# Performance work log

Measured on AMD Instinct MI355X. Metric: run time of the kernel, lower is better.

## Reference

```python
import jax, jax.numpy as jnp
import numpy as np

NEG = -1e9
SLOPE = 0.2  # LeakyReLU slope (GAT convention)


def setup_inputs() -> dict:
    key = jax.random.key(0)
    ks = jax.random.split(key, 10)
    T, N, E, F, Hd = 32, 512, 64, 64, 64
    x = jax.random.normal(ks[0], (T, N, F), dtype=jnp.float32)
    # Hyperedge incidence [N, E]; guarantee every node is in >= 1 hyperedge.
    Hm = (jax.random.uniform(ks[1], (N, E)) < (2.0 / E)).astype(jnp.int32)
    Hm = Hm.at[jnp.arange(N), jnp.arange(N) % E].set(1)
    # Industry adjacency [N, N] with self loops.
    adj = (jax.random.uniform(ks[2], (N, N)) < 0.05).astype(jnp.int32)
    adj = adj.at[jnp.arange(N), jnp.arange(N)].set(1)
    sc = 0.1
    W = jax.random.normal(ks[3], (F, Hd), jnp.float32) * sc
    a_hyp = jax.random.normal(ks[4], (Hd,), jnp.float32) * sc
    a_ind = jax.random.normal(ks[5], (Hd,), jnp.float32) * sc
    Wc1 = jax.random.normal(ks[6], (Hd, Hd), jnp.float32) * sc
    bc1 = jnp.zeros((Hd,), jnp.float32)
    wc2 = jax.random.normal(ks[7], (Hd,), jnp.float32) * sc
    bc2 = jnp.zeros((), jnp.float32)
    return dict(x=x, H=Hm, adj=adj, nhid=Hd, W=W, a_hyp=a_hyp, a_ind=a_ind,
                Wc1=Wc1, bc1=bc1, wc2=wc2, bc2=bc2)


def _edgeconv(feats, mask, Wc1, bc1, wc2, bc2):
    """Attention pooling over the second-to-last (set) axis.
    feats: [..., K, Hd], mask: broadcastable to [..., K] (bool). -> [..., Hd]"""
    z = jnp.maximum(feats @ Wc1 + bc1, 0.0) @ wc2 + bc2  # [..., K]
    z = jnp.where(mask, z, NEG)
    alpha = jax.nn.softmax(z, axis=-1)
    return jnp.einsum('...k,...kd->...d', alpha, feats)


def reference(x, H, adj, nhid, W, a_hyp, a_ind, Wc1, bc1, wc2, bc2):
    # x: [T, N, F]; H: [N, E] incidence; adj: [N, N]. Eval mode: dropout = id.
    Hb = H.astype(bool)          # [N, E]
    Ab = adj.astype(bool)        # [N, N]
    h = x @ W                    # [T, N, Hd]

    # --- hyperedge_attn: intra-hyperedge node attention (GAT-style) ---
    s_hyp = jax.nn.leaky_relu(h @ a_hyp, SLOPE)                 # [T, N]
    logits = jnp.where(Hb[None, :, :], s_hyp[:, :, None], NEG)  # [T, N, E]
    alpha = jax.nn.softmax(logits, axis=1)                      # over nodes in edge
    # per-(edge,node) contribution; original layout [E,T,N,Hd] -> here [T,N,E,Hd]
    all_hyper = jax.nn.elu(alpha[..., None] * h[:, :, None, :])  # [T, N, E, Hd]

    # --- industry attention over adj ---
    s_ind = jax.nn.leaky_relu(h @ a_ind, SLOPE)                   # [T, N]
    li = jnp.where(Ab[None, :, :], s_ind[:, None, :], NEG)        # [T, N, N]
    beta = jax.nn.softmax(li, axis=-1)
    industry = jnp.einsum('tij,tjd->tid', beta, h)                # [T, N, Hd]

    # --- per-node loop, vectorized ---
    # y8: EdgeConv over the hyperedges containing each node (mask = H row).
    # When a node has exactly 1 hyperedge, masked softmax selects it exactly,
    # which reproduces the original else-branch.
    y8 = _edgeconv(all_hyper, Hb[None, :, :], Wc1, bc1, wc2, bc2)  # [T, N, Hd]
    pair = jnp.stack([industry, y8], axis=2)                       # [T, N, 2, Hd]
    y9 = _edgeconv(pair, jnp.ones((1, 1, 2), bool), Wc1, bc1, wc2, bc2)
    return y9                                                      # [T, N, Hd]
```

## Files before the change

### kernel.cpp

```cpp
#include <hip/hip_runtime.h>

#define T_DIM 32
#define N_DIM 512
#define E_DIM 64
#define F_DIM 64
#define HD    64
#define NBR_CAP 128

static_assert(E_DIM == 64 && HD == 64 && F_DIM == 64, "wave-mapped dims");

__device__ __forceinline__ float wave_sum(float v) {
    #pragma unroll
    for (int off = 32; off > 0; off >>= 1) v += __shfl_xor(v, off, 64);
    return v;
}
__device__ __forceinline__ void wave_sum2(float& a, float& b) {
    #pragma unroll
    for (int off = 32; off > 0; off >>= 1) {
        a += __shfl_xor(a, off, 64);
        b += __shfl_xor(b, off, 64);
    }
}

#define K1_R 16
#define K1_ROWBLK (T_DIM * N_DIM / K1_R)
#define K1_CSRBLK (N_DIM / 4)
__global__ __launch_bounds__(256) void k1_h_s(
    const float* __restrict__ x, const float* __restrict__ W,
    const float* __restrict__ a_hyp, const float* __restrict__ a_ind,
    const int* __restrict__ adj, const int* __restrict__ Hm,
    float* __restrict__ h, float* __restrict__ s_hyp, float* __restrict__ s_ind,
    int* __restrict__ degs, int* __restrict__ nbrs, int* __restrict__ Ht)
{
    const int wave = threadIdx.x >> 6;
    const int lane = threadIdx.x & 63;

    if (blockIdx.x < K1_ROWBLK) {
        __shared__ float xl[K1_R * F_DIM];
        const int row0 = blockIdx.x * K1_R;
        ((float4*)xl)[threadIdx.x] =
            ((const float4*)(x + (size_t)row0 * F_DIM))[threadIdx.x];
        float wcol[F_DIM];
        #pragma unroll
        for (int f = 0; f < F_DIM; ++f) wcol[f] = W[f * HD + lane];
        const float ah = a_hyp[lane], ai = a_ind[lane];
        __syncthreads();
        #pragma unroll
        for (int r = wave; r < K1_R; r += 4) {
            float a0 = 0.f, a1 = 0.f, a2 = 0.f, a3 = 0.f;
            #pragma unroll
            for (int f = 0; f < F_DIM; f += 4) {
                const float4 xv = *(const float4*)&xl[r * F_DIM + f];
                a0 = fmaf(xv.x, wcol[f + 0], a0);
                a1 = fmaf(xv.y, wcol[f + 1], a1);
                a2 = fmaf(xv.z, wcol[f + 2], a2);
                a3 = fmaf(xv.w, wcol[f + 3], a3);
            }
            const float acc = (a0 + a1) + (a2 + a3);
            h[(size_t)(row0 + r) * HD + lane] = acc;
            float sh = acc * ah, si = acc * ai;
            wave_sum2(sh, si);
            if (lane == 0) {
                s_hyp[row0 + r] = sh > 0.f ? sh : 0.2f * sh;
                s_ind[row0 + r] = si > 0.f ? si : 0.2f * si;
            }
        }
    } else if (blockIdx.x < K1_ROWBLK + K1_CSRBLK) {
        const int i = (blockIdx.x - K1_ROWBLK) * 4 + wave;
        int deg = 0;
        #pragma unroll
        for (int c = 0; c < N_DIM / 64; ++c) {
            const int j = c * 64 + lane;
            const bool bit = adj[(size_t)i * N_DIM + j] != 0;
            const unsigned long long mask = __ballot(bit);
            if (bit) {
                const int pos = deg + __popcll(mask & ((1ull << lane) - 1ull));
                nbrs[i * NBR_CAP + pos] = j;
            }
            deg += __popcll(mask);
        }
        if (lane == 0) degs[i] = deg;
    } else {
        for (int idx = threadIdx.x; idx < N_DIM * E_DIM; idx += 256) {
            const int n = idx >> 6, e = idx & 63;
            Ht[e * N_DIM + n] = Hm[idx];
        }
    }
}

#define K2_BLOCKS (T_DIM * E_DIM / 4)
__global__ __launch_bounds__(256) void k23_stats_industry(
    const int* __restrict__ Ht, const int* __restrict__ degs,
    const int* __restrict__ nbrs,
    const float* __restrict__ s_hyp, const float* __restrict__ s_ind,
    const float* __restrict__ h,
    float* __restrict__ d_e, float* __restrict__ industry)
{
    const int wave = threadIdx.x >> 6;
    const int lane = threadIdx.x & 63;

    if (blockIdx.x < K2_BLOCKS) {
        const int idx = blockIdx.x * 4 + wave;
        const int t = idx >> 6, e = idx & 63;
        const int*   hrow = Ht + e * N_DIM;
        const float* srow = s_hyp + t * N_DIM;
        float sum = 0.f;
        #pragma unroll
        for (int c = 0; c < N_DIM / 64; ++c) {
            const int n = c * 64 + lane;
            if (hrow[n]) sum += expf(srow[n]);
        }
        sum = wave_sum(sum);
        if (lane == 0) d_e[idx] = sum;
    } else {
        const int idx = (blockIdx.x - K2_BLOCKS) * 4 + wave;
        const int t = idx >> 9, i = idx & (N_DIM - 1);
        const int deg = degs[i];
        const int* nb = nbrs + i * NBR_CAP;
        const float* st = s_ind + t * N_DIM;
        const float* hbase = h + (size_t)t * N_DIM * HD;
        float evp = 0.f, ac0 = 0.f, ac1 = 0.f, ac2 = 0.f, ac3 = 0.f;
        for (int base = 0; base < deg; base += 64) {
            const int k = base + lane;
            const bool valid = k < deg;
            const int j = valid ? nb[k] : 0;
            const float ev = valid ? expf(st[j]) : 0.f;
            evp += ev;
            const int cnt = min(deg - base, 64);
            int kk = 0;
            for (; kk + 4 <= cnt; kk += 4) {
                const int j0 = __shfl(j, kk, 64),     j1 = __shfl(j, kk + 1, 64);
                const int j2 = __shfl(j, kk + 2, 64), j3 = __shfl(j, kk + 3, 64);
                const float w0 = __shfl(ev, kk, 64),     w1 = __shfl(ev, kk + 1, 64);
                const float w2 = __shfl(ev, kk + 2, 64), w3 = __shfl(ev, kk + 3, 64);
                const float v0 = hbase[(size_t)j0 * HD + lane];
                const float v1 = hbase[(size_t)j1 * HD + lane];
                const float v2 = hbase[(size_t)j2 * HD + lane];
                const float v3 = hbase[(size_t)j3 * HD + lane];
                ac0 = fmaf(w0, v0, ac0);
                ac1 = fmaf(w1, v1, ac1);
                ac2 = fmaf(w2, v2, ac2);
                ac3 = fmaf(w3, v3, ac3);
            }
            for (; kk < cnt; ++kk) {
                const int jj = __shfl(j, kk, 64);
                const float ww = __shfl(ev, kk, 64);
                ac0 = fmaf(ww, hbase[(size_t)jj * HD + lane], ac0);
            }
        }
        const float evsum = wave_sum(evp);
        industry[(size_t)idx * HD + lane] = ((ac0 + ac1) + (ac2 + ac3)) / evsum;
    }
}

__global__ __launch_bounds__(256) void k4_final(
    const int* __restrict__ Hm, const float* __restrict__ s_hyp,
    const float* __restrict__ d_e,
    const float* __restrict__ h, const float* __restrict__ industry,
    const float* __restrict__ Wc1, const float* __restrict__ bc1,
    const float* __restrict__ wc2, const float* __restrict__ bc2,
    float* __restrict__ out)
{
    __shared__ float fl[4 * 2 * HD];
    const int wave = threadIdx.x >> 6;
    const int lane = threadIdx.x & 63;
    const int idx  = blockIdx.x * 4 + wave;
    const int t = idx >> 9, n = idx & (N_DIM - 1);
    float* fw = fl + wave * 2 * HD;

    float wreg[HD];
    #pragma unroll
    for (int d = 0; d < HD; ++d) wreg[d] = Wc1[d * HD + lane];
    const float bc1v = bc1[lane];
    const float wc2v = wc2[lane];
    const float bc2v = bc2[0];

    const float hv = h[(size_t)idx * HD + lane];
    const float esh = expf(s_hyp[idx]);

    const int memv = Hm[n * E_DIM + lane];
    const float alpha = memv ? esh * __frcp_rn(d_e[t * E_DIM + lane]) : 0.f;
    unsigned long long mk = __ballot(memv != 0);

    float zsum = 0.f, acc = 0.f;
    while (mk) {
        const int e0 = __ffsll((long long)mk) - 1; mk &= mk - 1;
        const bool have1 = mk != 0;
        const int e1 = have1 ? __ffsll((long long)mk) - 1 : e0;
        if (have1) mk &= mk - 1;
        const float a0 = __shfl(alpha, e0, 64);
        const float a1 = __shfl(alpha, e1, 64);
        float f0 = a0 * hv; f0 = f0 > 0.f ? f0 : expm1f(f0);
        float f1 = a1 * hv; f1 = f1 > 0.f ? f1 : expm1f(f1);
        fw[lane]      = f0;
        fw[HD + lane] = f1;
        float u0 = 0.f, u1 = 0.f, u2 = 0.f, u3 = 0.f;
        float v0 = 0.f, v1 = 0.f, v2 = 0.f, v3 = 0.f;
        #pragma unroll
        for (int d = 0; d < HD; d += 4) {
            const float4 A = *(const float4*)&fw[d];
            const float4 B = *(const float4*)&fw[HD + d];
            u0 = fmaf(A.x, wreg[d + 0], u0);
            u1 = fmaf(A.y, wreg[d + 1], u1);
            u2 = fmaf(A.z, wreg[d + 2], u2);
            u3 = fmaf(A.w, wreg[d + 3], u3);
            v0 = fmaf(B.x, wreg[d + 0], v0);
            v1 = fmaf(B.y, wreg[d + 1], v1);
            v2 = fmaf(B.z, wreg[d + 2], v2);
            v3 = fmaf(B.w, wreg[d + 3], v3);
        }
        float p = fmaxf((u0 + u1) + (u2 + u3) + bc1v, 0.f) * wc2v;
        float q = fmaxf((v0 + v1) + (v2 + v3) + bc1v, 0.f) * wc2v;
        wave_sum2(p, q);
        const float w0 = expf(p + bc2v);
        const float w1 = have1 ? expf(q + bc2v) : 0.f;
        zsum += w0 + w1;
        acc = fmaf(w0, f0, acc);
        acc = fmaf(w1, f1, acc);
    }
    const float y8 = acc / zsum;

    const float indv = industry[(size_t)idx * HD + lane];
    fw[lane]      = indv;
    fw[HD + lane] = y8;
    float p0 = 0.f, p1 = 0.f, q0 = 0.f, q1 = 0.f;
    #pragma unroll
    for (int d = 0; d < HD; d += 4) {
        const float4 iv = *(const float4*)&fw[d];
        const float4 yv = *(const float4*)&fw[HD + d];
        p0 = fmaf(iv.x, wreg[d + 0], p0);
        p1 = fmaf(iv.y, wreg[d + 1], p1);
        p0 = fmaf(iv.z, wreg[d + 2], p0);
        p1 = fmaf(iv.w, wreg[d + 3], p1);
        q0 = fmaf(yv.x, wreg[d + 0], q0);
        q1 = fmaf(yv.y, wreg[d + 1], q1);
        q0 = fmaf(yv.z, wreg[d + 2], q0);
        q1 = fmaf(yv.w, wreg[d + 3], q1);
    }
    float zp = fmaxf(p0 + p1 + bc1v, 0.f) * wc2v;
    float zq = fmaxf(q0 + q1 + bc1v, 0.f) * wc2v;
    wave_sum2(zp, zq);
    const float w0 = expf(zp + bc2v), w1 = expf(zq + bc2v);
    out[(size_t)idx * HD + lane] = fmaf(w0, indv, w1 * y8) / (w0 + w1);
}

extern "C" void kernel_launch(void* const* d_in, const int* in_sizes, int n_in,
                              void* d_out, int out_size, void* d_ws, size_t ws_size,
                              hipStream_t stream) {
    const float* x     = (const float*)d_in[0];
    const int*   Hm    = (const int*)  d_in[1];
    const int*   adj   = (const int*)  d_in[2];
    const float* W     = (const float*)d_in[4];
    const float* a_hyp = (const float*)d_in[5];
    const float* a_ind = (const float*)d_in[6];
    const float* Wc1   = (const float*)d_in[7];
    const float* bc1   = (const float*)d_in[8];
    const float* wc2   = (const float*)d_in[9];
    const float* bc2   = (const float*)d_in[10];
    float* out = (float*)d_out;

    float* ws       = (float*)d_ws;
    float* h        = ws;
    float* s_hyp    = h + (size_t)T_DIM * N_DIM * HD;
    float* s_ind    = s_hyp + T_DIM * N_DIM;
    float* d_e      = s_ind + T_DIM * N_DIM;
    float* industry = d_e + T_DIM * E_DIM;
    int*   degs     = (int*)(industry + (size_t)T_DIM * N_DIM * HD);
    int*   nbrs     = degs + N_DIM;
    int*   Ht       = nbrs + N_DIM * NBR_CAP;

    k1_h_s<<<K1_ROWBLK + K1_CSRBLK + 1, 256, 0, stream>>>(
        x, W, a_hyp, a_ind, adj, Hm, h, s_hyp, s_ind, degs, nbrs, Ht);
    k23_stats_industry<<<K2_BLOCKS + T_DIM * N_DIM / 4, 256, 0, stream>>>(
        Ht, degs, nbrs, s_hyp, s_ind, h, d_e, industry);
    k4_final<<<T_DIM * N_DIM / 4, 256, 0, stream>>>(
        Hm, s_hyp, d_e, h, industry, Wc1, bc1, wc2, bc2, out);
}
```

Baseline: 164.3 us.

## Drop H transpose block and compute hyperedge denominators per timestep with shared exps

Removes the single-block transpose of the incidence matrix, which was a serial tail in the first kernel. The hyperedge softmax denominators are now computed by one block per timestep that caches exp(s_hyp) in shared memory and reads H row-major with lanes mapped to edges. Each exp is then computed once per node instead of once per (edge,node), at the cost of only T blocks doing this work. It also raises rows per block in the h projection from 16 to 64, which amortises the per-thread loads of the W column.

```diff
diff --git a/kernel.cpp b/kernel.cpp
--- a/kernel.cpp
+++ b/kernel.cpp
@@ -22,15 +22,15 @@
     }
 }
 
-#define K1_R 16
+#define K1_R 64
 #define K1_ROWBLK (T_DIM * N_DIM / K1_R)
 #define K1_CSRBLK (N_DIM / 4)
 __global__ __launch_bounds__(256) void k1_h_s(
     const float* __restrict__ x, const float* __restrict__ W,
     const float* __restrict__ a_hyp, const float* __restrict__ a_ind,
-    const int* __restrict__ adj, const int* __restrict__ Hm,
+    const int* __restrict__ adj,
     float* __restrict__ h, float* __restrict__ s_hyp, float* __restrict__ s_ind,
-    int* __restrict__ degs, int* __restrict__ nbrs, int* __restrict__ Ht)
+    int* __restrict__ degs, int* __restrict__ nbrs)
 {
     const int wave = threadIdx.x >> 6;
     const int lane = threadIdx.x & 63;
@@ -38,8 +38,10 @@
     if (blockIdx.x < K1_ROWBLK) {
         __shared__ float xl[K1_R * F_DIM];
         const int row0 = blockIdx.x * K1_R;
-        ((float4*)xl)[threadIdx.x] =
-            ((const float4*)(x + (size_t)row0 * F_DIM))[threadIdx.x];
+        #pragma unroll
+        for (int c = 0; c < K1_R * F_DIM / 4 / 256; ++c)
+            ((float4*)xl)[c * 256 + threadIdx.x] =
+                ((const float4*)(x + (size_t)row0 * F_DIM))[c * 256 + threadIdx.x];
         float wcol[F_DIM];
         #pragma unroll
         for (int f = 0; f < F_DIM; ++f) wcol[f] = W[f * HD + lane];
@@ -65,7 +67,7 @@
                 s_ind[row0 + r] = si > 0.f ? si : 0.2f * si;
             }
         }
-    } else if (blockIdx.x < K1_ROWBLK + K1_CSRBLK) {
+    } else {
         const int i = (blockIdx.x - K1_ROWBLK) * 4 + wave;
         int deg = 0;
         #pragma unroll
@@ -80,17 +82,11 @@
             deg += __popcll(mask);
         }
         if (lane == 0) degs[i] = deg;
-    } else {
-        for (int idx = threadIdx.x; idx < N_DIM * E_DIM; idx += 256) {
-            const int n = idx >> 6, e = idx & 63;
-            Ht[e * N_DIM + n] = Hm[idx];
-        }
-    }
-}
-
-#define K2_BLOCKS (T_DIM * E_DIM / 4)
+    }
+}
+
 __global__ __launch_bounds__(256) void k23_stats_industry(
-    const int* __restrict__ Ht, const int* __restrict__ degs,
+    const int* __restrict__ Hm, const int* __restrict__ degs,
     const int* __restrict__ nbrs,
     const float* __restrict__ s_hyp, const float* __restrict__ s_ind,
     const float* __restrict__ h,
@@ -99,21 +95,29 @@
     const int wave = threadIdx.x >> 6;
     const int lane = threadIdx.x & 63;
 
-    if (blockIdx.x < K2_BLOCKS) {
-        const int idx = blockIdx.x * 4 + wave;
-        const int t = idx >> 6, e = idx & 63;
-        const int*   hrow = Ht + e * N_DIM;
-        const float* srow = s_hyp + t * N_DIM;
-        float sum = 0.f;
-        #pragma unroll
-        for (int c = 0; c < N_DIM / 64; ++c) {
-            const int n = c * 64 + lane;
-            if (hrow[n]) sum += expf(srow[n]);
-        }
-        sum = wave_sum(sum);
-        if (lane == 0) d_e[idx] = sum;
+    if (blockIdx.x < T_DIM) {
+        const int t = blockIdx.x;
+        __shared__ float exps[N_DIM];
+        __shared__ float departial[4][E_DIM];
+        #pragma unroll
+        for (int c = 0; c < N_DIM / 256; ++c)
+            exps[c * 256 + threadIdx.x] = expf(s_hyp[t * N_DIM + c * 256 + threadIdx.x]);
+        __syncthreads();
+        float de = 0.f;
+        const int n0 = wave * (N_DIM / 4);
+        #pragma unroll 4
+        for (int k = 0; k < N_DIM / 4; ++k) {
+            const int n = n0 + k;
+            const int m = Hm[n * E_DIM + lane];
+            de += m ? exps[n] : 0.f;
+        }
+        departial[wave][lane] = de;
+        __syncthreads();
+        if (wave == 0)
+            d_e[t * E_DIM + lane] = (departial[0][lane] + departial[1][lane])
+                                  + (departial[2][lane] + departial[3][lane]);
     } else {
-        const int idx = (blockIdx.x - K2_BLOCKS) * 4 + wave;
+        const int idx = (blockIdx.x - T_DIM) * 4 + wave;
         const int t = idx >> 9, i = idx & (N_DIM - 1);
         const int deg = degs[i];
         const int* nb = nbrs + i * NBR_CAP;
@@ -267,12 +271,11 @@
     float* industry = d_e + T_DIM * E_DIM;
     int*   degs     = (int*)(industry + (size_t)T_DIM * N_DIM * HD);
     int*   nbrs     = degs + N_DIM;
-    int*   Ht       = nbrs + N_DIM * NBR_CAP;
-
-    k1_h_s<<<K1_ROWBLK + K1_CSRBLK + 1, 256, 0, stream>>>(
-        x, W, a_hyp, a_ind, adj, Hm, h, s_hyp, s_ind, degs, nbrs, Ht);
-    k23_stats_industry<<<K2_BLOCKS + T_DIM * N_DIM / 4, 256, 0, stream>>>(
-        Ht, degs, nbrs, s_hyp, s_ind, h, d_e, industry);
+
+    k1_h_s<<<K1_ROWBLK + K1_CSRBLK, 256, 0, stream>>>(
+        x, W, a_hyp, a_ind, adj, h, s_hyp, s_ind, degs, nbrs);
+    k23_stats_industry<<<T_DIM + T_DIM * N_DIM / 4, 256, 0, stream>>>(
+        Hm, degs, nbrs, s_hyp, s_ind, h, d_e, industry);
     k4_final<<<T_DIM * N_DIM / 4, 256, 0, stream>>>(
         Hm, s_hyp, d_e, h, industry, Wc1, bc1, wc2, bc2, out);
 }
```

Result: no change. 161.6 us (-1.6%).
